# Kernel tuning notes

Hardware: AMD Instinct MI355X
Metric: run time of the kernel (lower is better)

## Reference

```python
import jax, jax.numpy as jnp
import numpy as np

B, S, D = 2, 2048, 1024
H = 16
HD = D // H
SCALE = float(np.sqrt(HD))


def setup_inputs() -> dict:
    key = jax.random.key(0)
    ks = jax.random.split(key, 10)
    def lin(k):
        # xavier_uniform for [out, in] = [D, D]
        bound = float(np.sqrt(6.0 / (D + D)))
        return jax.random.uniform(k, (D, D), jnp.float32, -bound, bound)
    return {
        "hidden_states": jax.random.normal(ks[0], (B, S, D), jnp.float32),
        "attention_mask": jnp.ones((B, S), jnp.float32),
        "Wq": lin(ks[1]), "bq": jnp.zeros((D,), jnp.float32),
        "Wk": lin(ks[2]), "bk": jnp.zeros((D,), jnp.float32),
        "Wv": lin(ks[3]), "bv": jnp.zeros((D,), jnp.float32),
        "Wo": lin(ks[4]), "bo": jnp.zeros((D,), jnp.float32),
    }


def _heads(x):
    # [B,S,D] -> [B,H,S,HD]
    return x.reshape(B, S, H, HD).transpose(0, 2, 1, 3)


def secure_softmax(scores):
    c = jnp.clip(scores, -3.0, 3.0)
    sig = 0.5 + 0.25 * c - 0.01 * c ** 3
    sig = jnp.clip(sig, 0.01, 0.99)
    return sig / (jnp.sum(sig, axis=-1, keepdims=True) + 1e-8)


def reference(hidden_states, attention_mask, Wq, bq, Wk, bk, Wv, bv, Wo, bo):
    q = _heads(hidden_states @ Wq.T + bq)
    k = _heads(hidden_states @ Wk.T + bk)
    v = _heads(hidden_states @ Wv.T + bv)
    # [B,H,S,S]
    scores = jnp.einsum("bhqd,bhkd->bhqk", q, k) / SCALE
    scores = scores + (1.0 - attention_mask[:, None, None, :]) * -10000.0
    probs = secure_softmax(scores)
    ctx = jnp.einsum("bhqk,bhkd->bhqd", probs, v)
    ctx = ctx.transpose(0, 2, 1, 3).reshape(B, S, D)
    return ctx @ Wo.T + bo
```

## Files before the change

### kernel.cpp

```cpp
#include <hip/hip_runtime.h>
#include <stdint.h>

#define B_ 2
#define S_ 2048
#define D_ 1024
#define H_ 16
#define HD_ 64
#define M_ (B_*S_)

typedef __bf16 bf16;
typedef __attribute__((ext_vector_type(8))) __bf16 bf16x8;
typedef __attribute__((ext_vector_type(4))) float f32x4;
typedef __attribute__((ext_vector_type(2))) float f32x2;

__device__ __forceinline__ void gload16(const bf16* g, bf16* l) {
    __builtin_amdgcn_global_load_lds(
        (const __attribute__((address_space(1))) void*)g,
        (__attribute__((address_space(3))) void*)l, 16, 0, 0);
}

__global__ void k_cvt_all(const float* __restrict__ hs,
                          const float* __restrict__ Wq, const float* __restrict__ Wk,
                          const float* __restrict__ Wv, const float* __restrict__ Wo,
                          bf16* __restrict__ hb,
                          bf16* __restrict__ wqb, bf16* __restrict__ wkb,
                          bf16* __restrict__ wvb, bf16* __restrict__ wob) {
    int blk = blockIdx.x;
    const float* s; bf16* d; int base;
    if (blk < 2048) { s = hs; d = hb; base = blk; }
    else {
        int r = blk - 2048; int which = r >> 9; base = r & 511;
        s = (which==0)?Wq:(which==1)?Wk:(which==2)?Wv:Wo;
        d = (which==0)?wqb:(which==1)?wkb:(which==2)?wvb:wob;
    }
    int idx = base*2048 + threadIdx.x*8;
    float4 a = *(const float4*)(s + idx);
    float4 b = *(const float4*)(s + idx + 4);
    bf16 o[8] = {(bf16)a.x,(bf16)a.y,(bf16)a.z,(bf16)a.w,
                 (bf16)b.x,(bf16)b.y,(bf16)b.z,(bf16)b.w};
    *(int4*)(d + idx) = *(const int4*)o;
}

__global__ __launch_bounds__(256) void k_gemm_qkv(
    const bf16* __restrict__ X,
    const bf16* __restrict__ Wq, const bf16* __restrict__ Wk, const bf16* __restrict__ Wv,
    const float* __restrict__ bq, const float* __restrict__ bk, const float* __restrict__ bv,
    bf16* __restrict__ Qo, bf16* __restrict__ Ko, bf16* __restrict__ Vo)
{
    const int z = blockIdx.z;
    const bf16* W = (z==0) ? Wq : (z==1) ? Wk : Wv;
    const float* bias = (z==0) ? bq : (z==1) ? bk : bv;
    const int n0 = blockIdx.x * 128;
    const int m0 = blockIdx.y * 128;
    const int t = threadIdx.x;
    const int w = t >> 6, lane = t & 63, quad = lane >> 4, l15 = lane & 15;
    const int lr = lane >> 3;
    const int lc = (lane & 7) ^ lr;
    const int sx = l15 & 7;
    const int mw = (w >> 1) * 64, nw = (w & 1) * 64;

    __shared__ __align__(16) char smraw[128*136*2];
    bf16* As  = (bf16*)smraw;
    bf16* Bs  = (bf16*)(smraw + 16384);
    bf16* epi = (bf16*)smraw;

    f32x4 acc[4][4];
    #pragma unroll
    for (int i = 0; i < 4; i++)
        #pragma unroll
        for (int j = 0; j < 4; j++)
            acc[i][j] = (f32x4){0.f,0.f,0.f,0.f};

    const bf16* gA = X + (size_t)(m0 + w*8 + lr)*D_ + lc*8;
    const bf16* gB = W + (size_t)(n0 + w*8 + lr)*D_ + lc*8;

    for (int k0 = 0; k0 < D_; k0 += 64) {
        #pragma unroll
        for (int c = 0; c < 4; c++) {
            gload16(gA + (size_t)c*32*D_ + k0, &As[c*2048 + w*512]);
            gload16(gB + (size_t)c*32*D_ + k0, &Bs[c*2048 + w*512]);
        }
        __syncthreads();
        #pragma unroll
        for (int ks = 0; ks < 2; ks++) {
            bf16x8 af[4], bfr[4];
            #pragma unroll
            for (int i = 0; i < 4; i++)
                af[i] = *(const bf16x8*)&As[(mw + i*16 + l15)*64 + (((ks*4+quad)^sx)*8)];
            #pragma unroll
            for (int j = 0; j < 4; j++)
                bfr[j] = *(const bf16x8*)&Bs[(nw + j*16 + l15)*64 + (((ks*4+quad)^sx)*8)];
            #pragma unroll
            for (int i = 0; i < 4; i++)
                #pragma unroll
                for (int j = 0; j < 4; j++)
                    acc[i][j] = __builtin_amdgcn_mfma_f32_16x16x32_bf16(af[i], bfr[j], acc[i][j], 0, 0, 0);
        }
        __syncthreads();
    }

    const float scale = (z == 0) ? 0.125f : 1.0f;
    if (z == 2) {
        #pragma unroll
        for (int j = 0; j < 4; j++) {
            int n = nw + j*16 + l15;
            float bn = bias[n0 + n];
            #pragma unroll
            for (int i = 0; i < 4; i++) {
                int mloc = mw + i*16 + quad*4;
                union { bf16 h4[4]; uint2 u; } pk;
                #pragma unroll
                for (int r = 0; r < 4; r++) pk.h4[r] = (bf16)(acc[i][j][r] + bn);
                *(uint2*)&epi[n*136 + mloc] = pk.u;
            }
        }
    } else {
        #pragma unroll
        for (int j = 0; j < 4; j++) {
            int n = nw + j*16 + l15;
            float bn = bias[n0 + n];
            #pragma unroll
            for (int i = 0; i < 4; i++) {
                int mloc = mw + i*16 + quad*4;
                #pragma unroll
                for (int r = 0; r < 4; r++)
                    epi[(mloc + r)*136 + n] = (bf16)((acc[i][j][r] + bn) * scale);
            }
        }
    }
    __syncthreads();
    if (z == 2) {
        #pragma unroll
        for (int kk = 0; kk < 8; kk++) {
            int c = t + 256*kk;
            int row = c >> 4;
            int mcol = (c & 15) * 8;
            int4 val = *(const int4*)&epi[row*136 + mcol];
            int n = n0 + row; int hh = n >> 6, hd = n & 63;
            int m = m0 + mcol; int bb = m >> 11, s = m & 2047;
            *(int4*)&Vo[((size_t)((bb*H_ + hh)*HD_ + hd))*S_ + s] = val;
        }
    } else {
        bf16* Out = (z == 0) ? Qo : Ko;
        #pragma unroll
        for (int kk = 0; kk < 8; kk++) {
            int c = t + 256*kk;
            int row = c >> 4;
            int ncol = (c & 15) * 8;
            int4 val = *(const int4*)&epi[row*136 + ncol];
            int m = m0 + row; int bb = m >> 11, s = m & 2047;
            int n = n0 + ncol; int hh = n >> 6, hd = n & 63;
            *(int4*)&Out[((size_t)((bb*H_ + hh)*S_ + s))*HD_ + hd] = val;
        }
    }
}

__global__ __launch_bounds__(256) void k_gemm_out(
    const bf16* __restrict__ X, const bf16* __restrict__ W,
    const float* __restrict__ bias, float* __restrict__ Out)
{
    const int n0 = blockIdx.x * 128;
    const int m0 = blockIdx.y * 64;
    const int t = threadIdx.x;
    const int w = t >> 6, lane = t & 63, quad = lane >> 4, l15 = lane & 15;
    const int lr = lane >> 3;
    const int lc = (lane & 7) ^ lr;
    const int sx = l15 & 7;
    const int nw = w * 32;

    __shared__ __align__(16) bf16 As[64*64];
    __shared__ __align__(16) bf16 Bs[128*64];

    f32x4 acc[4][2];
    #pragma unroll
    for (int i = 0; i < 4; i++)
        #pragma unroll
        for (int j = 0; j < 2; j++)
            acc[i][j] = (f32x4){0.f,0.f,0.f,0.f};

    const bf16* gA = X + (size_t)(m0 + w*8 + lr)*D_ + lc*8;
    const bf16* gB = W + (size_t)(n0 + w*8 + lr)*D_ + lc*8;

    for (int k0 = 0; k0 < D_; k0 += 64) {
        #pragma unroll
        for (int c = 0; c < 2; c++)
            gload16(gA + (size_t)c*32*D_ + k0, &As[c*2048 + w*512]);
        #pragma unroll
        for (int c = 0; c < 4; c++)
            gload16(gB + (size_t)c*32*D_ + k0, &Bs[c*2048 + w*512]);
        __syncthreads();
        #pragma unroll
        for (int ks = 0; ks < 2; ks++) {
            bf16x8 af[4], bfr[2];
            #pragma unroll
            for (int i = 0; i < 4; i++)
                af[i] = *(const bf16x8*)&As[(i*16 + l15)*64 + (((ks*4+quad)^sx)*8)];
            #pragma unroll
            for (int j = 0; j < 2; j++)
                bfr[j] = *(const bf16x8*)&Bs[(nw + j*16 + l15)*64 + (((ks*4+quad)^sx)*8)];
            #pragma unroll
            for (int i = 0; i < 4; i++)
                #pragma unroll
                for (int j = 0; j < 2; j++)
                    acc[i][j] = __builtin_amdgcn_mfma_f32_16x16x32_bf16(af[i], bfr[j], acc[i][j], 0, 0, 0);
        }
        __syncthreads();
    }

    #pragma unroll
    for (int j = 0; j < 2; j++) {
        int n = n0 + nw + j*16 + l15;
        float bn = bias[n];
        #pragma unroll
        for (int i = 0; i < 4; i++) {
            int mbase = m0 + i*16 + quad*4;
            #pragma unroll
            for (int r = 0; r < 4; r++)
                Out[(size_t)(mbase + r)*D_ + n] = acc[i][j][r] + bn;
        }
    }
}

__global__ __launch_bounds__(256, 2) void k_attn(
    const bf16* __restrict__ Q, const bf16* __restrict__ K, const bf16* __restrict__ Vt,
    const float* __restrict__ mask, bf16* __restrict__ Ctx)
{
    const int bh = blockIdx.y;
    const int b = bh >> 4, h = bh & 15;
    const int q0 = blockIdx.x * 128;
    const int t = threadIdx.x;
    const int w = t >> 6, lane = t & 63, quad = lane >> 4, l15 = lane & 15;
    const int lr = lane >> 3;
    const int lc = (lane & 7) ^ lr;
    const int sx = l15 & 7;

    __shared__ __align__(16) bf16 Ks[2][64*64];
    __shared__ __align__(16) bf16 Vs[2][64*64];
    __shared__ __align__(16) bf16 Ps[128*64];
    __shared__ float lsumP[4][128];

    bf16x8 qf[8][2];
    const bf16* Qbase = Q + ((size_t)bh*S_ + q0)*HD_;
    #pragma unroll
    for (int qs = 0; qs < 8; qs++)
        #pragma unroll
        for (int ks = 0; ks < 2; ks++)
            qf[qs][ks] = *(const bf16x8*)&Qbase[(size_t)(qs*16 + l15)*HD_ + ks*32 + quad*8];

    f32x4 cacc[2][4];
    #pragma unroll
    for (int i = 0; i < 2; i++)
        #pragma unroll
        for (int j = 0; j < 4; j++)
            cacc[i][j] = (f32x4){0.f,0.f,0.f,0.f};
    f32x2 lacv[8];
    #pragma unroll
    for (int qs = 0; qs < 8; qs++) lacv[qs] = (f32x2){0.f,0.f};

    const bf16* Kst = K + ((size_t)bh*S_ + w*8 + lr)*HD_ + lc*8;
    const bf16* Vst = Vt + ((size_t)bh*HD_ + w*8 + lr)*S_ + lc*8;
    const float* mrow = mask + (size_t)b*S_ + w*16 + quad*4;

    #pragma unroll
    for (int c = 0; c < 2; c++)
        gload16(Kst + (size_t)c*32*HD_, &Ks[0][c*2048 + w*512]);
    #pragma unroll
    for (int c = 0; c < 2; c++)
        gload16(Vst + (size_t)c*32*S_, &Vs[0][c*2048 + w*512]);
    float4 m4 = *(const float4*)&mrow[0];
    __syncthreads();

    for (int it = 0; it < S_/64; it++) {
        const int cur = it & 1;
        const int k0 = it*64;
        const int notlast = (it < S_/64 - 1);
        const int nxt = cur ^ 1, k1 = k0 + 64;

        float4 m4n;
        if (notlast) {
            #pragma unroll
            for (int c = 0; c < 2; c++)
                gload16(Kst + (size_t)(k1 + c*32)*HD_, &Ks[nxt][c*2048 + w*512]);
            m4n = *(const float4*)&mrow[k1];
        }

        f32x2 mv01 = (f32x2){m4.x, m4.y} * 10000.f - 10000.f;
        f32x2 mv23 = (f32x2){m4.z, m4.w} * 10000.f - 10000.f;
        const f32x4 stinit = {mv01.x, mv01.y, mv23.x, mv23.y};

        f32x4 st[8];
        #pragma unroll
        for (int qs = 0; qs < 8; qs++) st[qs] = stinit;
        #pragma unroll
        for (int ks = 0; ks < 2; ks++) {
            bf16x8 af = *(const bf16x8*)&Ks[cur][(w*16 + l15)*64 + (((ks*4+quad)^sx)*8)];
            __builtin_amdgcn_s_setprio(1);
            #pragma unroll
            for (int qs = 0; qs < 8; qs++)
                st[qs] = __builtin_amdgcn_mfma_f32_16x16x32_bf16(af, qf[qs][ks], st[qs], 0, 0, 0);
            __builtin_amdgcn_s_setprio(0);
        }

        const f32x2 vn3 = {-3.f, -3.f}, vp3 = {3.f, 3.f};
        const int c8 = (w*2 + (quad>>1)) ^ sx;
        #pragma unroll
        for (int qs = 0; qs < 8; qs++) {
            f32x2 lo = {st[qs][0], st[qs][1]};
            f32x2 hi = {st[qs][2], st[qs][3]};
            lo = __builtin_elementwise_min(__builtin_elementwise_max(lo, vn3), vp3);
            hi = __builtin_elementwise_min(__builtin_elementwise_max(hi, vn3), vp3);
            f32x2 ulo = lo * lo;
            f32x2 uhi = hi * hi;
            f32x2 tlo = ulo * (-0.01f) + 0.25f;
            f32x2 thi = uhi * (-0.01f) + 0.25f;
            f32x2 slo = lo * tlo + 0.5f;
            f32x2 shi = hi * thi + 0.5f;
            lacv[qs] += slo;
            lacv[qs] += shi;
            union { bf16 h4[4]; uint2 u; } pk;
            pk.h4[0] = (bf16)slo.x; pk.h4[1] = (bf16)slo.y;
            pk.h4[2] = (bf16)shi.x; pk.h4[3] = (bf16)shi.y;
            *(uint2*)&Ps[(qs*16 + l15)*64 + c8*8 + (quad&1)*4] = pk.u;
        }
        __syncthreads();

        if (notlast) {
            #pragma unroll
            for (int c = 0; c < 2; c++)
                gload16(Vst + (size_t)c*32*S_ + k1, &Vs[nxt][c*2048 + w*512]);
        }

        #pragma unroll
        for (int ks = 0; ks < 2; ks++) {
            bf16x8 pf[2], vf[4];
            #pragma unroll
            for (int m2 = 0; m2 < 2; m2++)
                pf[m2] = *(const bf16x8*)&Ps[(w*32 + m2*16 + l15)*64 + (((ks*4+quad)^sx)*8)];
            #pragma unroll
            for (int nt = 0; nt < 4; nt++)
                vf[nt] = *(const bf16x8*)&Vs[cur][(nt*16 + l15)*64 + (((ks*4+quad)^sx)*8)];
            __builtin_amdgcn_s_setprio(1);
            #pragma unroll
            for (int m2 = 0; m2 < 2; m2++)
                #pragma unroll
                for (int nt = 0; nt < 4; nt++)
                    cacc[m2][nt] = __builtin_amdgcn_mfma_f32_16x16x32_bf16(pf[m2], vf[nt], cacc[m2][nt], 0, 0, 0);
            __builtin_amdgcn_s_setprio(0);
        }
        __syncthreads();

        m4 = m4n;
    }

    #pragma unroll
    for (int qs = 0; qs < 8; qs++) {
        float v = lacv[qs].x + lacv[qs].y;
        v += __shfl_xor(v, 16);
        v += __shfl_xor(v, 32);
        if (quad == 0) lsumP[w][qs*16 + l15] = v;
    }
    __syncthreads();

    #pragma unroll
    for (int m2 = 0; m2 < 2; m2++) {
        #pragma unroll
        for (int r = 0; r < 4; r++) {
            int q = w*32 + m2*16 + quad*4 + r;
            float s = lsumP[0][q] + lsumP[1][q] + lsumP[2][q] + lsumP[3][q];
            float rinv = 1.0f / (s + 1e-8f);
            size_t row = (size_t)(b*S_ + q0 + q);
            #pragma unroll
            for (int nt = 0; nt < 4; nt++)
                Ctx[row*D_ + h*HD_ + nt*16 + l15] = (bf16)(cacc[m2][nt][r] * rinv);
        }
    }
}

extern "C" void kernel_launch(void* const* d_in, const int* in_sizes, int n_in,
                              void* d_out, int out_size, void* d_ws, size_t ws_size,
                              hipStream_t stream) {
    const float* hs   = (const float*)d_in[0];
    const float* mask = (const float*)d_in[1];
    const float* Wq   = (const float*)d_in[2];
    const float* bq   = (const float*)d_in[3];
    const float* Wk   = (const float*)d_in[4];
    const float* bk   = (const float*)d_in[5];
    const float* Wv   = (const float*)d_in[6];
    const float* bv   = (const float*)d_in[7];
    const float* Wo   = (const float*)d_in[8];
    const float* bo   = (const float*)d_in[9];
    float* out = (float*)d_out;

    char* ws = (char*)d_ws;
    const size_t MB = 1024*1024;
    bf16* hb   = (bf16*)(ws);
    bf16* wqb  = (bf16*)(ws + 8*MB);
    bf16* wkb  = (bf16*)(ws + 10*MB);
    bf16* wvb  = (bf16*)(ws + 12*MB);
    bf16* wob  = (bf16*)(ws + 14*MB);
    bf16* qb   = (bf16*)(ws + 16*MB);
    bf16* kb   = (bf16*)(ws + 24*MB);
    bf16* vtb  = (bf16*)(ws + 32*MB);
    bf16* ctxb = (bf16*)(ws + 40*MB);

    k_cvt_all<<<2048 + 4*512, 256, 0, stream>>>(hs, Wq, Wk, Wv, Wo, hb, wqb, wkb, wvb, wob);

    k_gemm_qkv<<<dim3(D_/128, M_/128, 3), 256, 0, stream>>>(
        hb, wqb, wkb, wvb, bq, bk, bv, qb, kb, vtb);

    k_attn<<<dim3(S_/128, B_*H_), 256, 0, stream>>>(qb, kb, vtb, mask, ctxb);

    k_gemm_out<<<dim3(D_/128, M_/64), 256, 0, stream>>>(ctxb, wob, bo, out);
}
```

Before: 210.7 us.

## Keep attention probabilities in registers, drop LDS P round-trip

```diff
diff --git a/kernel.cpp b/kernel.cpp
--- a/kernel.cpp
+++ b/kernel.cpp
@@ -231,21 +231,21 @@
     const int t = threadIdx.x;
     const int w = t >> 6, lane = t & 63, quad = lane >> 4, l15 = lane & 15;
     const int lr = lane >> 3;
-    const int lc = (lane & 7) ^ lr;
+    const int lcV = (lane & 7) ^ lr;
+    const int lcK = (lane & 7) ^ ((lr & 3) | ((w & 1) << 2));
     const int sx = l15 & 7;
+    const int arow = ((l15 & 12) << 1) | (l15 & 3);
 
     __shared__ __align__(16) bf16 Ks[2][64*64];
     __shared__ __align__(16) bf16 Vs[2][64*64];
-    __shared__ __align__(16) bf16 Ps[128*64];
-    __shared__ float lsumP[4][128];
-
-    bf16x8 qf[8][2];
-    const bf16* Qbase = Q + ((size_t)bh*S_ + q0)*HD_;
-    #pragma unroll
-    for (int qs = 0; qs < 8; qs++)
+
+    bf16x8 qf[2][2];
+    const bf16* Qbase = Q + ((size_t)bh*S_ + q0 + w*32)*HD_;
+    #pragma unroll
+    for (int m2 = 0; m2 < 2; m2++)
         #pragma unroll
         for (int ks = 0; ks < 2; ks++)
-            qf[qs][ks] = *(const bf16x8*)&Qbase[(size_t)(qs*16 + l15)*HD_ + ks*32 + quad*8];
+            qf[m2][ks] = *(const bf16x8*)&Qbase[(size_t)(m2*16 + l15)*HD_ + ks*32 + quad*8];
 
     f32x4 cacc[2][4];
     #pragma unroll
@@ -253,122 +253,129 @@
         #pragma unroll
         for (int j = 0; j < 4; j++)
             cacc[i][j] = (f32x4){0.f,0.f,0.f,0.f};
-    f32x2 lacv[8];
-    #pragma unroll
-    for (int qs = 0; qs < 8; qs++) lacv[qs] = (f32x2){0.f,0.f};
-
-    const bf16* Kst = K + ((size_t)bh*S_ + w*8 + lr)*HD_ + lc*8;
-    const bf16* Vst = Vt + ((size_t)bh*HD_ + w*8 + lr)*S_ + lc*8;
-    const float* mrow = mask + (size_t)b*S_ + w*16 + quad*4;
+    f32x2 lacv[2];
+    #pragma unroll
+    for (int m2 = 0; m2 < 2; m2++) lacv[m2] = (f32x2){0.f,0.f};
+
+    const bf16* KstK = K  + ((size_t)bh*S_  + w*8 + lr)*HD_ + lcK*8;
+    const bf16* VstV = Vt + ((size_t)bh*HD_ + w*8 + lr)*S_  + lcV*8;
+    const float* mrow = mask + (size_t)b*S_ + quad*8;
 
     #pragma unroll
     for (int c = 0; c < 2; c++)
-        gload16(Kst + (size_t)c*32*HD_, &Ks[0][c*2048 + w*512]);
+        gload16(KstK + (size_t)c*32*HD_, &Ks[0][c*2048 + w*512]);
     #pragma unroll
     for (int c = 0; c < 2; c++)
-        gload16(Vst + (size_t)c*32*S_, &Vs[0][c*2048 + w*512]);
-    float4 m4 = *(const float4*)&mrow[0];
+        gload16(VstV + (size_t)c*32*S_, &Vs[0][c*2048 + w*512]);
+    float4 m4[4], m4n[4];
+    #pragma unroll
+    for (int g = 0; g < 4; g++)
+        m4[g] = *(const float4*)&mrow[(g>>1)*32 + (g&1)*4];
     __syncthreads();
 
     for (int it = 0; it < S_/64; it++) {
-        const int cur = it & 1;
-        const int k0 = it*64;
-        const int notlast = (it < S_/64 - 1);
-        const int nxt = cur ^ 1, k1 = k0 + 64;
-
-        float4 m4n;
+        const int cur = it & 1, nxt = cur ^ 1;
+        const int k1 = it*64 + 64;
+        const bool notlast = (it < S_/64 - 1);
+
         if (notlast) {
             #pragma unroll
             for (int c = 0; c < 2; c++)
-                gload16(Kst + (size_t)(k1 + c*32)*HD_, &Ks[nxt][c*2048 + w*512]);
-            m4n = *(const float4*)&mrow[k1];
-        }
-
-        f32x2 mv01 = (f32x2){m4.x, m4.y} * 10000.f - 10000.f;
-        f32x2 mv23 = (f32x2){m4.z, m4.w} * 10000.f - 10000.f;
-        const f32x4 stinit = {mv01.x, mv01.y, mv23.x, mv23.y};
-
-        f32x4 st[8];
-        #pragma unroll
-        for (int qs = 0; qs < 8; qs++) st[qs] = stinit;
+                gload16(KstK + (size_t)(k1 + c*32)*HD_, &Ks[nxt][c*2048 + w*512]);
+            #pragma unroll
+            for (int c = 0; c < 2; c++)
+                gload16(VstV + (size_t)c*32*S_ + k1, &Vs[nxt][c*2048 + w*512]);
+            #pragma unroll
+            for (int g = 0; g < 4; g++)
+                m4n[g] = *(const float4*)&mrow[k1 + (g>>1)*32 + (g&1)*4];
+        }
+
+        f32x4 st[4][2];
+        #pragma unroll
+        for (int g = 0; g < 4; g++) {
+            f32x4 sti = (f32x4){m4[g].x, m4[g].y, m4[g].z, m4[g].w} * 10000.f - 10000.f;
+            st[g][0] = sti;
+            st[g][1] = sti;
+        }
+
+        __builtin_amdgcn_s_setprio(1);
         #pragma unroll
         for (int ks = 0; ks < 2; ks++) {
-            bf16x8 af = *(const bf16x8*)&Ks[cur][(w*16 + l15)*64 + (((ks*4+quad)^sx)*8)];
+            #pragma unroll
+            for (int g = 0; g < 4; g++) {
+                const int kk = g >> 1, hf = g & 1;
+                bf16x8 af = *(const bf16x8*)&Ks[cur][(arow + hf*4 + kk*32)*64 + (((ks*4+quad)^sx)*8)];
+                #pragma unroll
+                for (int m2 = 0; m2 < 2; m2++)
+                    st[g][m2] = __builtin_amdgcn_mfma_f32_16x16x32_bf16(af, qf[m2][ks], st[g][m2], 0, 0, 0);
+            }
+        }
+        __builtin_amdgcn_s_setprio(0);
+
+        const f32x2 vn3 = {-3.f, -3.f}, vp3 = {3.f, 3.f};
+        bf16x8 pa[2][2];
+        #pragma unroll
+        for (int m2 = 0; m2 < 2; m2++) {
+            #pragma unroll
+            for (int kk = 0; kk < 2; kk++) {
+                union { bf16 h8[8]; bf16x8 v; } pk;
+                #pragma unroll
+                for (int hf = 0; hf < 2; hf++) {
+                    f32x4 sv = st[kk*2 + hf][m2];
+                    f32x2 lo = {sv[0], sv[1]};
+                    f32x2 hi = {sv[2], sv[3]};
+                    lo = __builtin_elementwise_min(__builtin_elementwise_max(lo, vn3), vp3);
+                    hi = __builtin_elementwise_min(__builtin_elementwise_max(hi, vn3), vp3);
+                    f32x2 tlo = lo * lo * (-0.01f) + 0.25f;
+                    f32x2 thi = hi * hi * (-0.01f) + 0.25f;
+                    f32x2 slo = lo * tlo + 0.5f;
+                    f32x2 shi = hi * thi + 0.5f;
+                    lacv[m2] += slo;
+                    lacv[m2] += shi;
+                    pk.h8[hf*4+0] = (bf16)slo.x; pk.h8[hf*4+1] = (bf16)slo.y;
+                    pk.h8[hf*4+2] = (bf16)shi.x; pk.h8[hf*4+3] = (bf16)shi.y;
+                }
+                pa[m2][kk] = pk.v;
+            }
+        }
+
+        #pragma unroll
+        for (int kk = 0; kk < 2; kk++) {
+            bf16x8 vf[4];
+            #pragma unroll
+            for (int nt = 0; nt < 4; nt++)
+                vf[nt] = *(const bf16x8*)&Vs[cur][(nt*16 + l15)*64 + (((kk*4+quad)^sx)*8)];
             __builtin_amdgcn_s_setprio(1);
             #pragma unroll
-            for (int qs = 0; qs < 8; qs++)
-                st[qs] = __builtin_amdgcn_mfma_f32_16x16x32_bf16(af, qf[qs][ks], st[qs], 0, 0, 0);
+            for (int m2 = 0; m2 < 2; m2++)
+                #pragma unroll
+                for (int nt = 0; nt < 4; nt++)
+                    cacc[m2][nt] = __builtin_amdgcn_mfma_f32_16x16x32_bf16(pa[m2][kk], vf[nt], cacc[m2][nt], 0, 0, 0);
             __builtin_amdgcn_s_setprio(0);
         }
 
-        const f32x2 vn3 = {-3.f, -3.f}, vp3 = {3.f, 3.f};
-        const int c8 = (w*2 + (quad>>1)) ^ sx;
-        #pragma unroll
-        for (int qs = 0; qs < 8; qs++) {
-            f32x2 lo = {st[qs][0], st[qs][1]};
-            f32x2 hi = {st[qs][2], st[qs][3]};
-            lo = __builtin_elementwise_min(__builtin_elementwise_max(lo, vn3), vp3);
-            hi = __builtin_elementwise_min(__builtin_elementwise_max(hi, vn3), vp3);
-            f32x2 ulo = lo * lo;
-            f32x2 uhi = hi * hi;
-            f32x2 tlo = ulo * (-0.01f) + 0.25f;
-            f32x2 thi = uhi * (-0.01f) + 0.25f;
-            f32x2 slo = lo * tlo + 0.5f;
-            f32x2 shi = hi * thi + 0.5f;
-            lacv[qs] += slo;
-            lacv[qs] += shi;
-            union { bf16 h4[4]; uint2 u; } pk;
-            pk.h4[0] = (bf16)slo.x; pk.h4[1] = (bf16)slo.y;
-            pk.h4[2] = (bf16)shi.x; pk.h4[3] = (bf16)shi.y;
-            *(uint2*)&Ps[(qs*16 + l15)*64 + c8*8 + (quad&1)*4] = pk.u;
-        }
         __syncthreads();
 
-        if (notlast) {
-            #pragma unroll
-            for (int c = 0; c < 2; c++)
-                gload16(Vst + (size_t)c*32*S_ + k1, &Vs[nxt][c*2048 + w*512]);
-        }
-
-        #pragma unroll
-        for (int ks = 0; ks < 2; ks++) {
-            bf16x8 pf[2], vf[4];
-            #pragma unroll
-            for (int m2 = 0; m2 < 2; m2++)
-                pf[m2] = *(const bf16x8*)&Ps[(w*32 + m2*16 + l15)*64 + (((ks*4+quad)^sx)*8)];
-            #pragma unroll
-            for (int nt = 0; nt < 4; nt++)
-                vf[nt] = *(const bf16x8*)&Vs[cur][(nt*16 + l15)*64 + (((ks*4+quad)^sx)*8)];
-            __builtin_amdgcn_s_setprio(1);
-            #pragma unroll
-            for (int m2 = 0; m2 < 2; m2++)
-                #pragma unroll
-                for (int nt = 0; nt < 4; nt++)
-                    cacc[m2][nt] = __builtin_amdgcn_mfma_f32_16x16x32_bf16(pf[m2], vf[nt], cacc[m2][nt], 0, 0, 0);
-            __builtin_amdgcn_s_setprio(0);
-        }
-        __syncthreads();
-
-        m4 = m4n;
-    }
-
-    #pragma unroll
-    for (int qs = 0; qs < 8; qs++) {
-        float v = lacv[qs].x + lacv[qs].y;
+        #pragma unroll
+        for (int g = 0; g < 4; g++) m4[g] = m4n[g];
+    }
+
+    float s[2];
+    #pragma unroll
+    for (int m2 = 0; m2 < 2; m2++) {
+        float v = lacv[m2].x + lacv[m2].y;
         v += __shfl_xor(v, 16);
         v += __shfl_xor(v, 32);
-        if (quad == 0) lsumP[w][qs*16 + l15] = v;
-    }
-    __syncthreads();
+        s[m2] = v;
+    }
 
     #pragma unroll
     for (int m2 = 0; m2 < 2; m2++) {
         #pragma unroll
         for (int r = 0; r < 4; r++) {
-            int q = w*32 + m2*16 + quad*4 + r;
-            float s = lsumP[0][q] + lsumP[1][q] + lsumP[2][q] + lsumP[3][q];
-            float rinv = 1.0f / (s + 1e-8f);
-            size_t row = (size_t)(b*S_ + q0 + q);
+            float rs = __shfl(s[m2], quad*4 + r);
+            float rinv = 1.0f / (rs + 1e-8f);
+            size_t row = (size_t)(b*S_ + q0 + w*32 + m2*16 + quad*4 + r);
             #pragma unroll
             for (int nt = 0; nt < 4; nt++)
                 Ctx[row*D_ + h*HD_ + nt*16 + l15] = (bf16)(cacc[m2][nt][r] * rinv);
```

Measured after the change: 199.8 us. -5.2%, faster.
